# Kernel tuning notes

Hardware: AMD Instinct MI355X
Metric: run time of the kernel (lower is better)

The kernel has to match this reference:

```python
import jax, jax.numpy as jnp
import numpy as np

B, S, HID = 1, 2048, 4096
NH, NKV, HD = 32, 8, 128          # num_heads, num_key_value_heads, head_dim
N_REP = NH // NKV                  # GQA group size
ROPE_BASE = 10000.0


def rotate_half(x):
    x1, x2 = jnp.split(x, 2, axis=-1)
    return jnp.concatenate([-x2, x1], axis=-1)


def setup_inputs() -> dict:
    key = jax.random.key(0)
    k_hs, k_q, k_k, k_v, k_o = jax.random.split(key, 5)
    hidden_states = jax.random.normal(k_hs, (B, S, HID), dtype=jnp.float32)
    scale = 0.02
    wq = jax.random.normal(k_q, (HID, NH * HD), dtype=jnp.float32) * scale
    wk = jax.random.normal(k_k, (HID, NKV * HD), dtype=jnp.float32) * scale
    wv = jax.random.normal(k_v, (HID, NKV * HD), dtype=jnp.float32) * scale
    wo = jax.random.normal(k_o, (NH * HD, HID), dtype=jnp.float32) * scale
    # additive causal mask, 0 on/below diagonal, large negative above
    causal = jnp.tril(jnp.ones((S, S), dtype=bool))
    attention_mask = jnp.where(causal, 0.0, -1e9).astype(jnp.float32)[None, None]
    # RoPE cos/sin cache (LlamaRotaryEmbedding)
    inv_freq = 1.0 / (ROPE_BASE ** (jnp.arange(0, HD, 2, dtype=jnp.float32) / HD))
    t = jnp.arange(S, dtype=jnp.float32)
    freqs = jnp.outer(t, inv_freq)                 # [S, HD/2]
    emb = jnp.concatenate([freqs, freqs], axis=-1)  # [S, HD]
    cos, sin = jnp.cos(emb), jnp.sin(emb)
    return {"hidden_states": hidden_states, "attention_mask": attention_mask,
            "wq": wq, "wk": wk, "wv": wv, "wo": wo, "cos": cos, "sin": sin}


def reference(hidden_states, attention_mask, wq, wk, wv, wo, cos, sin):
    b, s, _ = hidden_states.shape
    # projections -> [b, heads, s, head_dim]
    q = (hidden_states @ wq).reshape(b, s, NH, HD).transpose(0, 2, 1, 3)
    k = (hidden_states @ wk).reshape(b, s, NKV, HD).transpose(0, 2, 1, 3)
    v = (hidden_states @ wv).reshape(b, s, NKV, HD).transpose(0, 2, 1, 3)
    # RoPE: cos/sin [s, hd] broadcast over batch and heads
    c = cos[None, None, :, :]
    sn = sin[None, None, :, :]
    q = q * c + rotate_half(q) * sn
    k = k * c + rotate_half(k) * sn
    # GQA repeat_kv: [b, nkv, s, d] -> [b, nh, s, d]
    k = jnp.repeat(k, N_REP, axis=1)
    v = jnp.repeat(v, N_REP, axis=1)
    scores = jnp.einsum('bhqd,bhkd->bhqk', q, k) / jnp.sqrt(jnp.float32(HD))
    scores = scores + attention_mask
    attn = jax.nn.softmax(scores.astype(jnp.float32), axis=-1).astype(q.dtype)
    out = jnp.einsum('bhqk,bhkd->bhqd', attn, v)        # [b, nh, s, d]
    out = out.transpose(0, 2, 1, 3).reshape(b, s, NH * HD)
    return out @ wo
```

## Files before the change

### kernel.cpp

```cpp
#include <hip/hip_runtime.h>


typedef __bf16 bf16_t;
typedef bf16_t bf16x8_t __attribute__((ext_vector_type(8)));
typedef float f32x4_t __attribute__((ext_vector_type(4)));

#define S_LEN 2048
#define HID 4096
#define NH 32
#define NKV 8
#define HD 128
#define KV_DIM 1024
#define QKV_DIM 6144
#define SCALE 0.08838834764831845f

__device__ __align__(16) bf16_t g_hsb[(size_t)S_LEN * HID];
__device__ __align__(16) bf16_t g_wqkvT[(size_t)QKV_DIM * HID];
__device__ __align__(16) bf16_t g_woT[(size_t)HID * HID];
__device__ __align__(16) bf16_t g_qkv[(size_t)S_LEN * QKV_DIM];
__device__ __align__(16) bf16_t g_vT[(size_t)NKV * HD * S_LEN];
__device__ __align__(16) bf16_t g_ao[(size_t)S_LEN * HID];

__device__ __forceinline__ void gl_lds16(const bf16_t* g, bf16_t* l) {
  __builtin_amdgcn_global_load_lds(
      (const __attribute__((address_space(1))) void*)g,
      (__attribute__((address_space(3))) void*)l, 16, 0, 0);
}

__global__ __launch_bounds__(256) void cast_f32_bf16(
    const float* __restrict__ in, bf16_t* __restrict__ out)
{
  size_t i = ((size_t)blockIdx.x * 256 + threadIdx.x) * 8;
  float4 a = *(const float4*)(in + i);
  float4 b = *(const float4*)(in + i + 4);
  bf16x8_t r;
  r[0] = (bf16_t)a.x; r[1] = (bf16_t)a.y; r[2] = (bf16_t)a.z; r[3] = (bf16_t)a.w;
  r[4] = (bf16_t)b.x; r[5] = (bf16_t)b.y; r[6] = (bf16_t)b.z; r[7] = (bf16_t)b.w;
  *(bf16x8_t*)(out + i) = r;
}

__global__ __launch_bounds__(256) void transpose_f32_bf16(
    const float* __restrict__ in, bf16_t* __restrict__ out, int is, int os)
{
  __shared__ __align__(16) bf16_t T[64 * 72];
  int r0 = blockIdx.x * 64, c0 = blockIdx.y * 64;
  int t = threadIdx.x;
#pragma unroll
  for (int it = 0; it < 2; ++it) {
    int idx = t + it * 256;
    int r = idx >> 3, c8 = (idx & 7) * 8;
    const float* p = in + (size_t)(r0 + r) * is + c0 + c8;
    float4 a = *(const float4*)p;
    float4 b = *(const float4*)(p + 4);
    bf16x8_t x;
    x[0] = (bf16_t)a.x; x[1] = (bf16_t)a.y; x[2] = (bf16_t)a.z; x[3] = (bf16_t)a.w;
    x[4] = (bf16_t)b.x; x[5] = (bf16_t)b.y; x[6] = (bf16_t)b.z; x[7] = (bf16_t)b.w;
    *(bf16x8_t*)(T + r * 72 + c8) = x;
  }
  __syncthreads();
#pragma unroll
  for (int it = 0; it < 2; ++it) {
    int idx = t + it * 256;
    int c = idx >> 3, r8 = (idx & 7) * 8;
    bf16x8_t x;
#pragma unroll
    for (int i = 0; i < 8; ++i) x[i] = T[(r8 + i) * 72 + c];
    *(bf16x8_t*)(out + (size_t)(c0 + c) * os + r0 + r8) = x;
  }
}

__global__ __launch_bounds__(256) void transpose_bf16(
    const bf16_t* __restrict__ in, bf16_t* __restrict__ out,
    int is, int os, int in_b, int out_b)
{
  __shared__ __align__(16) bf16_t T[64 * 72];
  const bf16_t* inp = in + (size_t)blockIdx.z * in_b;
  bf16_t* outp = out + (size_t)blockIdx.z * out_b;
  int r0 = blockIdx.x * 64, c0 = blockIdx.y * 64;
  int t = threadIdx.x;
#pragma unroll
  for (int it = 0; it < 2; ++it) {
    int idx = t + it * 256;
    int r = idx >> 3, c8 = (idx & 7) * 8;
    *(bf16x8_t*)(T + r * 72 + c8) =
        *(const bf16x8_t*)(inp + (size_t)(r0 + r) * is + c0 + c8);
  }
  __syncthreads();
#pragma unroll
  for (int it = 0; it < 2; ++it) {
    int idx = t + it * 256;
    int c = idx >> 3, r8 = (idx & 7) * 8;
    bf16x8_t x;
#pragma unroll
    for (int i = 0; i < 8; ++i) x[i] = T[(r8 + i) * 72 + c];
    *(bf16x8_t*)(outp + (size_t)(c0 + c) * os + r0 + r8) = x;
  }
}

#define VM4 asm volatile("s_waitcnt vmcnt(4)" ::: "memory")
#define VM0 asm volatile("s_waitcnt vmcnt(0)" ::: "memory")
#define SCHB __builtin_amdgcn_sched_barrier(0)
#define SBAR __builtin_amdgcn_s_barrier()

#define STAGE_A(tau, h)                                                     \
  { bf16_t* d_ = lds + (((tau) & 1) << 15) + (h) * 8192 + swb;              \
    const bf16_t* g_ = Ags + (size_t)((h) * 128) * K + (tau) * 64;          \
    gl_lds16(g_, d_); gl_lds16(g_ + (size_t)64 * K, d_ + 4096); }
#define STAGE_B(tau, h)                                                     \
  { bf16_t* d_ = lds + (((tau) & 1) << 15) + 16384 + (h) * 8192 + swb;      \
    const bf16_t* g_ = Bgs + (size_t)((h) * 128) * K + (tau) * 64;          \
    gl_lds16(g_, d_); gl_lds16(g_ + (size_t)64 * K, d_ + 4096); }

#define GPHASE(BUF, Q, STAGES, ENDSYNC)                                     \
  {                                                                         \
    if ((Q) == 0) {                                                         \
      _Pragma("unroll")                                                     \
      for (int ni = 0; ni < 4; ++ni) {                                      \
        bq[ni][0] = *(const bf16x8_t*)((BUF) + boff + ni * 2048 + colb0);   \
        bq[ni][1] = *(const bf16x8_t*)((BUF) + boff + ni * 2048 + colb1);   \
      }                                                                     \
    }                                                                       \
    bf16x8_t a00 = *(const bf16x8_t*)((BUF) + aoff + (2*(Q)) * 2048 + colb0);   \
    bf16x8_t a01 = *(const bf16x8_t*)((BUF) + aoff + (2*(Q)) * 2048 + colb1);   \
    bf16x8_t a10 = *(const bf16x8_t*)((BUF) + aoff + (2*(Q)+1) * 2048 + colb0); \
    bf16x8_t a11 = *(const bf16x8_t*)((BUF) + aoff + (2*(Q)+1) * 2048 + colb1); \
    STAGES;                                                                 \
    SBAR;                                                                   \
    asm volatile("s_waitcnt lgkmcnt(0)" ::: "memory");                      \
    SCHB;                                                                   \
    __builtin_amdgcn_s_setprio(1);                                          \
    _Pragma("unroll")                                                       \
    for (int ni = 0; ni < 4; ++ni) {                                        \
      acc[2*(Q)][ni]   = __builtin_amdgcn_mfma_f32_16x16x32_bf16(a00, bq[ni][0], acc[2*(Q)][ni],   0, 0, 0); \
      acc[2*(Q)][ni]   = __builtin_amdgcn_mfma_f32_16x16x32_bf16(a01, bq[ni][1], acc[2*(Q)][ni],   0, 0, 0); \
      acc[2*(Q)+1][ni] = __builtin_amdgcn_mfma_f32_16x16x32_bf16(a10, bq[ni][0], acc[2*(Q)+1][ni], 0, 0, 0); \
      acc[2*(Q)+1][ni] = __builtin_amdgcn_mfma_f32_16x16x32_bf16(a11, bq[ni][1], acc[2*(Q)+1][ni], 0, 0, 0); \
    }                                                                       \
    __builtin_amdgcn_s_setprio(0);                                          \
    ENDSYNC;                                                                \
  }

template <typename CT>
__global__ __launch_bounds__(512, 2) void gemm256(
    const bf16_t* __restrict__ A, const bf16_t* __restrict__ Bt,
    CT* __restrict__ C, int K, int N)
{
  __shared__ __align__(16) bf16_t lds[2 * 32768];
  const int t = threadIdx.x;
  const int wid = t >> 6, lane = t & 63;
  const int ln = lane & 15, lq = lane >> 4;
  const int wm = wid >> 2, wn = wid & 3;
  const int m0 = blockIdx.x * 256, n0 = blockIdx.y * 256;

  const int lx = (ln & 7) << 4;
  const int colb0 = (lq * 16) ^ lx;
  const int colb1 = (64 + lq * 16) ^ lx;
  const int aoff = wm * 16384 + ln * 128;
  const int boff = 32768 + (wn >> 1) * 16384 + ((wn & 1) * 64 + ln) * 128;

  const int srow = t >> 3;
  const int scol = ((((t & 7) * 16) ^ ((srow & 7) << 4)) >> 1);
  const int swb = wid * 512;
  const bf16_t* Ags = A + (size_t)(m0 + srow) * K + scol;
  const bf16_t* Bgs = Bt + (size_t)(n0 + srow) * K + scol;

  f32x4_t acc[8][4] = {};
  bf16x8_t bq[4][2];
  const char* const bufE = (const char*)lds;
  const char* const bufO = (const char*)lds + 65536;
  const int NITER = K >> 7;

  STAGE_A(0, 0) STAGE_A(0, 1) STAGE_B(0, 0) STAGE_B(0, 1)
  STAGE_B(1, 0) STAGE_B(1, 1)
  VM4;
  SCHB;
  SBAR;

  for (int I = 0; I < NITER; ++I) {
    const bool stg = (I + 1 < NITER);
    const int tb = 2 * I;
    GPHASE(bufE, 0, STAGE_A(tb + 1, 0), SBAR)
    GPHASE(bufE, 1, STAGE_A(tb + 1, 1), SBAR)
    GPHASE(bufE, 2, if (stg) STAGE_B(tb + 2, 0), SBAR)
    GPHASE(bufE, 3, if (stg) STAGE_B(tb + 2, 1),
           { if (stg) { VM4; } else { VM0; } SCHB; SBAR; })
    GPHASE(bufO, 0, if (stg) STAGE_A(tb + 2, 0), SBAR)
    GPHASE(bufO, 1, if (stg) STAGE_A(tb + 2, 1), SBAR)
    GPHASE(bufO, 2, if (stg) STAGE_B(tb + 3, 0), SBAR)
    GPHASE(bufO, 3, if (stg) STAGE_B(tb + 3, 1),
           { if (stg) { VM4; SCHB; } SBAR; })
  }

#pragma unroll
  for (int mi = 0; mi < 8; ++mi)
#pragma unroll
    for (int ni = 0; ni < 4; ++ni)
#pragma unroll
      for (int r = 0; r < 4; ++r)
        C[(size_t)(m0 + wm * 128 + mi * 16 + lq * 4 + r) * N
          + n0 + wn * 64 + ni * 16 + ln] = (CT)acc[mi][ni][r];
}

__global__ __launch_bounds__(256) void rope_kernel(
    bf16_t* __restrict__ qkv, const float* __restrict__ cs,
    const float* __restrict__ sn)
{
  int idx = blockIdx.x * 256 + threadIdx.x;
  int d = idx & 63;
  int h = (idx >> 6) % (NH + NKV);
  int s = idx / (64 * (NH + NKV));
  float c = cs[s * HD + d], si = sn[s * HD + d];
  bf16_t* base = qkv + (size_t)s * QKV_DIM +
                 ((h < NH) ? h * HD : HID + (h - NH) * HD);
  float x1 = (float)base[d], x2 = (float)base[d + 64];
  base[d]      = (bf16_t)(x1 * c - x2 * si);
  base[d + 64] = (bf16_t)(x2 * c + x1 * si);
}

__global__ __launch_bounds__(256) void attn_kernel(
    const bf16_t* __restrict__ QKV, const bf16_t* __restrict__ VT,
    bf16_t* __restrict__ O)
{
  __shared__ __align__(16) bf16_t Ks[64 * 136];
  __shared__ __align__(16) bf16_t Vs[128 * 72];
  __shared__ __align__(16) bf16_t Ps[4 * 16 * 72];
  int t = threadIdx.x, wave = t >> 6, lane = t & 63;
  int ln = lane & 15, lq = lane >> 4;
  int bid = blockIdx.x;
  int qb = (S_LEN / 64 - 1) - (bid >> 5);
  int head = bid & 31, kvh = head >> 2;
  int q0 = qb * 64;
  int qr = q0 + wave * 16 + ln;

  bf16x8_t qf[4];
#pragma unroll
  for (int kk = 0; kk < 4; ++kk)
    qf[kk] = *(const bf16x8_t*)(QKV + (size_t)qr * QKV_DIM + head * HD +
                                kk * 32 + lq * 8);

  f32x4_t oa[8] = {};
  float m_r[4] = {-1e30f, -1e30f, -1e30f, -1e30f};
  float l_r[4] = {0.f, 0.f, 0.f, 0.f};

  int krow = t >> 4, kdc = (t & 15) * 8;
  int vrow = t >> 3, vkc = (t & 7) * 8;
  const bf16_t* Kg = QKV + HID + (size_t)kvh * HD;
  const bf16_t* Vg = VT + (size_t)kvh * HD * S_LEN;

  for (int kt = 0; kt <= qb; ++kt) {
    int kb = kt * 64;
    __syncthreads();
#pragma unroll
    for (int p = 0; p < 4; ++p) {
      int r_ = p * 16 + krow;
      *(bf16x8_t*)(Ks + r_ * 136 + kdc) =
          *(const bf16x8_t*)(Kg + (size_t)(kb + r_) * QKV_DIM + kdc);
      int d_ = p * 32 + vrow;
      *(bf16x8_t*)(Vs + d_ * 72 + vkc) =
          *(const bf16x8_t*)(Vg + (size_t)d_ * S_LEN + kb + vkc);
    }
    __syncthreads();

    f32x4_t sv[4] = {};
#pragma unroll
    for (int nt = 0; nt < 4; ++nt)
#pragma unroll
      for (int kk = 0; kk < 4; ++kk) {
        bf16x8_t kf = *(const bf16x8_t*)(Ks + (nt * 16 + ln) * 136 +
                                         kk * 32 + lq * 8);
        sv[nt] = __builtin_amdgcn_mfma_f32_16x16x32_bf16(qf[kk], kf, sv[nt],
                                                         0, 0, 0);
      }

    float p_[4][4];
    if (kt == qb) {
#pragma unroll
      for (int nt = 0; nt < 4; ++nt)
#pragma unroll
        for (int r = 0; r < 4; ++r) {
          int rq = wave * 16 + lq * 4 + r;
          p_[nt][r] = (nt * 16 + ln <= rq) ? sv[nt][r] * SCALE : -1e30f;
        }
    } else {
#pragma unroll
      for (int nt = 0; nt < 4; ++nt)
#pragma unroll
        for (int r = 0; r < 4; ++r) p_[nt][r] = sv[nt][r] * SCALE;
    }

    float mx[4];
#pragma unroll
    for (int r = 0; r < 4; ++r)
      mx[r] = fmaxf(fmaxf(p_[0][r], p_[1][r]), fmaxf(p_[2][r], p_[3][r]));
#pragma unroll
    for (int off = 8; off >= 1; off >>= 1)
#pragma unroll
      for (int r = 0; r < 4; ++r) mx[r] = fmaxf(mx[r], __shfl_xor(mx[r], off, 64));

    float al[4], rs[4];
#pragma unroll
    for (int r = 0; r < 4; ++r) {
      float mn = fmaxf(m_r[r], mx[r]);
      al[r] = __expf(m_r[r] - mn);
      m_r[r] = mn;
      rs[r] = 0.f;
#pragma unroll
      for (int nt = 0; nt < 4; ++nt) {
        p_[nt][r] = __expf(p_[nt][r] - mn);
        rs[r] += p_[nt][r];
      }
    }
#pragma unroll
    for (int off = 8; off >= 1; off >>= 1)
#pragma unroll
      for (int r = 0; r < 4; ++r) rs[r] += __shfl_xor(rs[r], off, 64);
#pragma unroll
    for (int r = 0; r < 4; ++r) l_r[r] = l_r[r] * al[r] + rs[r];
#pragma unroll
    for (int dt = 0; dt < 8; ++dt)
#pragma unroll
      for (int r = 0; r < 4; ++r) oa[dt][r] *= al[r];

    bf16_t* myP = Ps + wave * 16 * 72;
#pragma unroll
    for (int nt = 0; nt < 4; ++nt)
#pragma unroll
      for (int r = 0; r < 4; ++r)
        myP[(lq * 4 + r) * 72 + nt * 16 + ln] = (bf16_t)p_[nt][r];
    bf16x8_t pf0 = *(const bf16x8_t*)(myP + ln * 72 + lq * 8);
    bf16x8_t pf1 = *(const bf16x8_t*)(myP + ln * 72 + 32 + lq * 8);
#pragma unroll
    for (int dt = 0; dt < 8; ++dt) {
      bf16x8_t v0 = *(const bf16x8_t*)(Vs + (dt * 16 + ln) * 72 + lq * 8);
      bf16x8_t v1 = *(const bf16x8_t*)(Vs + (dt * 16 + ln) * 72 + 32 + lq * 8);
      oa[dt] = __builtin_amdgcn_mfma_f32_16x16x32_bf16(pf0, v0, oa[dt], 0, 0, 0);
      oa[dt] = __builtin_amdgcn_mfma_f32_16x16x32_bf16(pf1, v1, oa[dt], 0, 0, 0);
    }
  }

#pragma unroll
  for (int dt = 0; dt < 8; ++dt)
#pragma unroll
    for (int r = 0; r < 4; ++r) {
      int row = q0 + wave * 16 + lq * 4 + r;
      O[(size_t)row * HID + head * HD + dt * 16 + ln] =
          (bf16_t)(oa[dt][r] / l_r[r]);
    }
}

extern "C" void kernel_launch(void* const* d_in, const int* in_sizes, int n_in,
                              void* d_out, int out_size, void* d_ws, size_t ws_size,
                              hipStream_t stream)
{
  (void)in_sizes; (void)n_in; (void)out_size; (void)d_ws; (void)ws_size;
  const float* hs = (const float*)d_in[0];
  const float* wq = (const float*)d_in[2];
  const float* wk = (const float*)d_in[3];
  const float* wv = (const float*)d_in[4];
  const float* wo = (const float*)d_in[5];
  const float* cs = (const float*)d_in[6];
  const float* sn = (const float*)d_in[7];
  float* out = (float*)d_out;

  bf16_t *hsb, *wqkvT, *woT, *qkv, *vT, *ao;
  hipGetSymbolAddress((void**)&hsb,   HIP_SYMBOL(g_hsb));
  hipGetSymbolAddress((void**)&wqkvT, HIP_SYMBOL(g_wqkvT));
  hipGetSymbolAddress((void**)&woT,   HIP_SYMBOL(g_woT));
  hipGetSymbolAddress((void**)&qkv,   HIP_SYMBOL(g_qkv));
  hipGetSymbolAddress((void**)&vT,    HIP_SYMBOL(g_vT));
  hipGetSymbolAddress((void**)&ao,    HIP_SYMBOL(g_ao));

  cast_f32_bf16<<<(S_LEN * HID) / (256 * 8), 256, 0, stream>>>(hs, hsb);

  transpose_f32_bf16<<<dim3(64, 64), 256, 0, stream>>>(wq, wqkvT, HID, HID);
  transpose_f32_bf16<<<dim3(64, 16), 256, 0, stream>>>(
      wk, wqkvT + (size_t)HID * HID, KV_DIM, HID);
  transpose_f32_bf16<<<dim3(64, 16), 256, 0, stream>>>(
      wv, wqkvT + (size_t)(HID + KV_DIM) * HID, KV_DIM, HID);
  transpose_f32_bf16<<<dim3(64, 64), 256, 0, stream>>>(wo, woT, HID, HID);

  gemm256<bf16_t><<<dim3(S_LEN / 256, QKV_DIM / 256), 512, 0, stream>>>(
      hsb, wqkvT, qkv, HID, QKV_DIM);

  rope_kernel<<<(S_LEN * (NH + NKV) * 64) / 256, 256, 0, stream>>>(qkv, cs, sn);

  transpose_bf16<<<dim3(S_LEN / 64, HD / 64, NKV), 256, 0, stream>>>(
      qkv + HID + KV_DIM, vT, QKV_DIM, S_LEN, HD, HD * S_LEN);

  attn_kernel<<<dim3((S_LEN / 64) * NH), 256, 0, stream>>>(qkv, vT, ao);

  gemm256<float><<<dim3(S_LEN / 256, HID / 256), 512, 0, stream>>>(
      ao, woT, out, HID, HID);
}
```

Measured before the change: 589.6 us.

## Fuse input cast and weight transposes into one prep kernel; reorder GEMM phase sync

Merges the hidden-state cast and the four weight transpose launches into a single kernel that dispatches on block index, removing four launches and the tail gaps between them. Separately, the GEMM phase macro now issues the async global-to-LDS staging and the barrier before the LDS fragment reads, and drops the explicit lgkmcnt wait and sched barrier so the compiler can interleave LDS reads with MFMAs. The second change alters the synchronisation and may expose LDS hazards or race timing, since the barrier now comes before the reads instead of after.

```diff
diff --git a/kernel.cpp b/kernel.cpp
--- a/kernel.cpp
+++ b/kernel.cpp
@@ -27,24 +27,10 @@
       (__attribute__((address_space(3))) void*)l, 16, 0, 0);
 }
 
-__global__ __launch_bounds__(256) void cast_f32_bf16(
-    const float* __restrict__ in, bf16_t* __restrict__ out)
-{
-  size_t i = ((size_t)blockIdx.x * 256 + threadIdx.x) * 8;
-  float4 a = *(const float4*)(in + i);
-  float4 b = *(const float4*)(in + i + 4);
-  bf16x8_t r;
-  r[0] = (bf16_t)a.x; r[1] = (bf16_t)a.y; r[2] = (bf16_t)a.z; r[3] = (bf16_t)a.w;
-  r[4] = (bf16_t)b.x; r[5] = (bf16_t)b.y; r[6] = (bf16_t)b.z; r[7] = (bf16_t)b.w;
-  *(bf16x8_t*)(out + i) = r;
-}
-
-__global__ __launch_bounds__(256) void transpose_f32_bf16(
-    const float* __restrict__ in, bf16_t* __restrict__ out, int is, int os)
-{
-  __shared__ __align__(16) bf16_t T[64 * 72];
-  int r0 = blockIdx.x * 64, c0 = blockIdx.y * 64;
-  int t = threadIdx.x;
+__device__ __forceinline__ void transpose_body(
+    const float* __restrict__ in, bf16_t* __restrict__ out,
+    int is, int os, int r0, int c0, int t, bf16_t* T)
+{
 #pragma unroll
   for (int it = 0; it < 2; ++it) {
     int idx = t + it * 256;
@@ -69,6 +55,39 @@
   }
 }
 
+__global__ __launch_bounds__(256) void prep_kernel(
+    const float* __restrict__ hs, const float* __restrict__ wq,
+    const float* __restrict__ wk, const float* __restrict__ wv,
+    const float* __restrict__ wo, bf16_t* __restrict__ hsb,
+    bf16_t* __restrict__ wqkvT, bf16_t* __restrict__ woT)
+{
+  __shared__ __align__(16) bf16_t T[64 * 72];
+  int bid = blockIdx.x, t = threadIdx.x;
+  if (bid < 4096) {
+    size_t i = ((size_t)bid * 256 + t) * 8;
+    float4 a = *(const float4*)(hs + i);
+    float4 b = *(const float4*)(hs + i + 4);
+    bf16x8_t r;
+    r[0] = (bf16_t)a.x; r[1] = (bf16_t)a.y; r[2] = (bf16_t)a.z; r[3] = (bf16_t)a.w;
+    r[4] = (bf16_t)b.x; r[5] = (bf16_t)b.y; r[6] = (bf16_t)b.z; r[7] = (bf16_t)b.w;
+    *(bf16x8_t*)(hsb + i) = r;
+  } else if (bid < 8192) {
+    int b = bid - 4096;
+    transpose_body(wq, wqkvT, HID, HID, (b & 63) * 64, (b >> 6) * 64, t, T);
+  } else if (bid < 9216) {
+    int b = bid - 8192;
+    transpose_body(wk, wqkvT + (size_t)HID * HID, KV_DIM, HID,
+                   (b & 63) * 64, (b >> 6) * 64, t, T);
+  } else if (bid < 10240) {
+    int b = bid - 9216;
+    transpose_body(wv, wqkvT + (size_t)(HID + KV_DIM) * HID, KV_DIM, HID,
+                   (b & 63) * 64, (b >> 6) * 64, t, T);
+  } else {
+    int b = bid - 10240;
+    transpose_body(wo, woT, HID, HID, (b & 63) * 64, (b >> 6) * 64, t, T);
+  }
+}
+
 __global__ __launch_bounds__(256) void transpose_bf16(
     const bf16_t* __restrict__ in, bf16_t* __restrict__ out,
     int is, int os, int in_b, int out_b)
@@ -113,6 +132,8 @@
 
 #define GPHASE(BUF, Q, STAGES, ENDSYNC)                                     \
   {                                                                         \
+    STAGES;                                                                 \
+    SBAR;                                                                   \
     if ((Q) == 0) {                                                         \
       _Pragma("unroll")                                                     \
       for (int ni = 0; ni < 4; ++ni) {                                      \
@@ -124,10 +145,6 @@
     bf16x8_t a01 = *(const bf16x8_t*)((BUF) + aoff + (2*(Q)) * 2048 + colb1);   \
     bf16x8_t a10 = *(const bf16x8_t*)((BUF) + aoff + (2*(Q)+1) * 2048 + colb0); \
     bf16x8_t a11 = *(const bf16x8_t*)((BUF) + aoff + (2*(Q)+1) * 2048 + colb1); \
-    STAGES;                                                                 \
-    SBAR;                                                                   \
-    asm volatile("s_waitcnt lgkmcnt(0)" ::: "memory");                      \
-    SCHB;                                                                   \
     __builtin_amdgcn_s_setprio(1);                                          \
     _Pragma("unroll")                                                       \
     for (int ni = 0; ni < 4; ++ni) {                                        \
@@ -370,14 +387,7 @@
   hipGetSymbolAddress((void**)&vT,    HIP_SYMBOL(g_vT));
   hipGetSymbolAddress((void**)&ao,    HIP_SYMBOL(g_ao));
 
-  cast_f32_bf16<<<(S_LEN * HID) / (256 * 8), 256, 0, stream>>>(hs, hsb);
-
-  transpose_f32_bf16<<<dim3(64, 64), 256, 0, stream>>>(wq, wqkvT, HID, HID);
-  transpose_f32_bf16<<<dim3(64, 16), 256, 0, stream>>>(
-      wk, wqkvT + (size_t)HID * HID, KV_DIM, HID);
-  transpose_f32_bf16<<<dim3(64, 16), 256, 0, stream>>>(
-      wv, wqkvT + (size_t)(HID + KV_DIM) * HID, KV_DIM, HID);
-  transpose_f32_bf16<<<dim3(64, 64), 256, 0, stream>>>(wo, woT, HID, HID);
+  prep_kernel<<<14336, 256, 0, stream>>>(hs, wq, wk, wv, wo, hsb, wqkvT, woT);
 
   gemm256<bf16_t><<<dim3(S_LEN / 256, QKV_DIM / 256), 512, 0, stream>>>(
       hsb, wqkvT, qkv, HID, QKV_DIM);
```

Measured after the change: 587.8 us. About the same (-0.3%).
